# Optimization experiments

Measured on AMD Instinct MI355X. Metric: run time of the kernel, lower is better.

## Reference

```python
import jax, jax.numpy as jnp
import numpy as np

NEG = -1000000.0  # mask fill value used by the torch module

def setup_inputs() -> dict:
    key = jax.random.key(0)
    ks = jax.random.split(key, 7)
    B, Tq, Tk, Din, H, Dv = 16, 128, 256, 64, 256, 256
    return {
        "queries": jax.random.normal(ks[0], (B, Tq, Din), dtype=jnp.float32),
        "keys": jax.random.normal(ks[1], (B, Tk, Din), dtype=jnp.float32),
        "values": jax.random.normal(ks[2], (B, Tk, Dv), dtype=jnp.float32),
        "valid_lens": jax.random.randint(ks[3], (B,), 0, Tk, dtype=jnp.int32),
        "wq": jax.random.normal(ks[4], (Din, H), dtype=jnp.float32) * 0.05,
        "wk": jax.random.normal(ks[5], (Din, H), dtype=jnp.float32) * 0.05,
        "wv": jax.random.normal(ks[6], (H,), dtype=jnp.float32) * 0.05,
    }

def reference(queries, keys, values, valid_lens, wq, wk, wv):
    # Project queries and keys to num_hiddens
    q = jnp.einsum("bqd,dh->bqh", queries, wq)       # [B,Tq,H]
    k = jnp.einsum("bkd,dh->bkh", keys, wk)          # [B,Tk,H]
    # Additive features [B,Tq,Tk,H] -> tanh -> scalar score via wv
    feats = jnp.tanh(q[:, :, None, :] + k[:, None, :, :])
    scores = jnp.einsum("bqkh,h->bqk", feats, wv)    # [B,Tq,Tk]
    # Masked softmax over last axis; valid_lens [B] broadcasts over Tq
    Tk = scores.shape[-1]
    mask = jnp.arange(Tk)[None, None, :] < valid_lens[:, None, None]
    scores = jnp.where(mask, scores, NEG)
    attn = jax.nn.softmax(scores, axis=-1)           # [B,Tq,Tk]
    return jnp.einsum("bqk,bkv->bqv", attn, values)  # [B,Tq,Dv]
```

## Files before the change

kernel.cpp:

```cpp
#include <hip/hip_runtime.h>

#define B_  16
#define TQ  128
#define TK  256
#define DIN 64
#define H_  256
#define DV  256
#define HT  8
#define QT  4
#define NW  8
#define NEG -1000000.0f

#define SCALE  2.8853900817779268f
#define LOG2E  1.4426950408889634f

__device__ inline float fast_exp2(float x) { return __builtin_amdgcn_exp2f(x); }
__device__ inline float fast_rcp(float x)  { return __builtin_amdgcn_rcpf(x); }

__global__ __launch_bounds__(256) void proj_k_kernel(
    const float* __restrict__ keys, const float* __restrict__ wk,
    float* __restrict__ kpT, const int* __restrict__ valid_lens)
{
    int b  = blockIdx.x >> 5;
    int h0 = (blockIdx.x & 31) * HT;
    int t  = threadIdx.x;
    int vlC = (valid_lens[b] + 63) & ~63;
    if (t >= vlC) return;
    const float* krow = keys + (b * TK + t) * DIN;
    float acc[HT];
    #pragma unroll
    for (int hh = 0; hh < HT; ++hh) acc[hh] = 0.f;
    #pragma unroll 4
    for (int d = 0; d < DIN; ++d) {
        float kv = krow[d];
        #pragma unroll
        for (int hh = 0; hh < HT; ++hh)
            acc[hh] = fmaf(kv, wk[d * H_ + h0 + hh], acc[hh]);
    }
    #pragma unroll
    for (int hh = 0; hh < HT; ++hh)
        kpT[(b * H_ + h0 + hh) * TK + t] = acc[hh] * SCALE;
}

__device__ inline float waveMax(float v) {
    #pragma unroll
    for (int off = 32; off > 0; off >>= 1) v = fmaxf(v, __shfl_xor(v, off, 64));
    return v;
}
__device__ inline float waveSum(float v) {
    #pragma unroll
    for (int off = 32; off > 0; off >>= 1) v += __shfl_xor(v, off, 64);
    return v;
}

#define ROW4(qr, sacc)                                            \
    {                                                             \
        float u0 = (qr) + kv.x, u1 = (qr) + kv.y;                 \
        float u2 = (qr) + kv.z, u3 = (qr) + kv.w;                 \
        float r0 = fast_rcp(fast_exp2(u0) + 1.f);                 \
        float r1 = fast_rcp(fast_exp2(u1) + 1.f);                 \
        float r2 = fast_rcp(fast_exp2(u2) + 1.f);                 \
        float r3 = fast_rcp(fast_exp2(u3) + 1.f);                 \
        sacc.x = fmaf(wvh, fmaf(-2.f, r0, 1.f), sacc.x);          \
        sacc.y = fmaf(wvh, fmaf(-2.f, r1, 1.f), sacc.y);          \
        sacc.z = fmaf(wvh, fmaf(-2.f, r2, 1.f), sacc.z);          \
        sacc.w = fmaf(wvh, fmaf(-2.f, r3, 1.f), sacc.w);          \
    }

__global__ __launch_bounds__(512) void attn_kernel(
    const float* __restrict__ queries, const float* __restrict__ wq,
    const float* __restrict__ kpT,
    const float* __restrict__ values, const int* __restrict__ valid_lens,
    const float* __restrict__ wv, float* __restrict__ out)
{
    __shared__ float2 qs2[2][H_];
    __shared__ float  wvL[H_];
    __shared__ float  scoreP[NW][QT][TK];
    __shared__ float  attnT[TK][QT];

    int bx = blockIdx.x;
    int xcd = bx & 7;
    int i   = bx >> 3;
    int b   = xcd + 8 * (i & 1);
    int q0  = (i >> 1) * QT;
    int t   = threadIdx.x;
    int w   = t >> 6, l = t & 63;
    int vl  = valid_lens[b];

    {
        int h = t & 255, rp = t >> 8;
        const float* qbase = queries + (b * TQ + q0 + rp * 2) * DIN;
        float a0 = 0.f, a1 = 0.f;
        #pragma unroll
        for (int d = 0; d < DIN; ++d) {
            float ww = wq[d * H_ + h];
            a0 = fmaf(qbase[d],       ww, a0);
            a1 = fmaf(qbase[DIN + d], ww, a1);
        }
        qs2[rp][h] = make_float2(a0 * SCALE, a1 * SCALE);
        if (t < 256) wvL[h] = wv[h];
    }
    __syncthreads();

    {
        const float4* kp4 = (const float4*)(kpT + (size_t)b * H_ * TK);
        float4 s0 = {0,0,0,0}, s1 = {0,0,0,0}, s2 = {0,0,0,0}, s3 = {0,0,0,0};
        int h0 = w * (H_ / NW);
        #pragma unroll 2
        for (int hh = 0; hh < H_ / NW; ++hh) {
            int h = h0 + hh;
            float4 kv  = kp4[h * (TK / 4) + l];
            float2 qA  = qs2[0][h];
            float2 qB  = qs2[1][h];
            float  wvh = wvL[h];
            ROW4(qA.x, s0);
            ROW4(qA.y, s1);
            ROW4(qB.x, s2);
            ROW4(qB.y, s3);
        }
        ((float4*)&scoreP[w][0][0])[l] = s0;
        ((float4*)&scoreP[w][1][0])[l] = s1;
        ((float4*)&scoreP[w][2][0])[l] = s2;
        ((float4*)&scoreP[w][3][0])[l] = s3;
    }
    __syncthreads();

    if (t < 64 * QT) {
        int r = w;
        float4 v = {0,0,0,0};
        #pragma unroll
        for (int s = 0; s < NW; ++s) {
            float4 ps = ((const float4*)&scoreP[s][r][0])[l];
            v.x += ps.x; v.y += ps.y; v.z += ps.z; v.w += ps.w;
        }
        int k0 = 4 * l;
        v.x = (k0     < vl) ? v.x : NEG;
        v.y = (k0 + 1 < vl) ? v.y : NEG;
        v.z = (k0 + 2 < vl) ? v.z : NEG;
        v.w = (k0 + 3 < vl) ? v.w : NEG;
        float m  = waveMax(fmaxf(fmaxf(v.x, v.y), fmaxf(v.z, v.w)));
        float p0 = fast_exp2((v.x - m) * LOG2E);
        float p1 = fast_exp2((v.y - m) * LOG2E);
        float p2 = fast_exp2((v.z - m) * LOG2E);
        float p3 = fast_exp2((v.w - m) * LOG2E);
        float dr = fast_rcp(waveSum(p0 + p1 + p2 + p3));
        attnT[k0    ][r] = p0 * dr;
        attnT[k0 + 1][r] = p1 * dr;
        attnT[k0 + 2][r] = p2 * dr;
        attnT[k0 + 3][r] = p3 * dr;
    }
    __syncthreads();

    {
        int half = t >> 8, v = t & 255;
        int kLim = (vl == 0) ? TK : vl;
        int kBeg = half * (TK / 2);
        int kEnd = min(kBeg + TK / 2, kLim);
        const float*  vcol = values + (size_t)b * TK * DV + v;
        const float4* at4  = (const float4*)attnT;
        float o0 = 0.f, o1 = 0.f, o2 = 0.f, o3 = 0.f;
        #pragma unroll 4
        for (int k = kBeg; k < kEnd; ++k) {
            float  vv = vcol[k * DV];
            float4 a  = at4[k];
            o0 = fmaf(a.x, vv, o0);
            o1 = fmaf(a.y, vv, o1);
            o2 = fmaf(a.z, vv, o2);
            o3 = fmaf(a.w, vv, o3);
        }
        if (half == 1) {
            scoreP[0][0][v] = o0;
            scoreP[0][1][v] = o1;
            scoreP[0][2][v] = o2;
            scoreP[0][3][v] = o3;
        }
        __syncthreads();
        if (half == 0) {
            float* orow = out + (size_t)(b * TQ + q0) * DV + v;
            orow[0]      = o0 + scoreP[0][0][v];
            orow[DV]     = o1 + scoreP[0][1][v];
            orow[2 * DV] = o2 + scoreP[0][2][v];
            orow[3 * DV] = o3 + scoreP[0][3][v];
        }
    }
}

extern "C" void kernel_launch(void* const* d_in, const int* in_sizes, int n_in,
                              void* d_out, int out_size, void* d_ws, size_t ws_size,
                              hipStream_t stream) {
    const float* queries    = (const float*)d_in[0];
    const float* keys       = (const float*)d_in[1];
    const float* values     = (const float*)d_in[2];
    const int*   valid_lens = (const int*)  d_in[3];
    const float* wq         = (const float*)d_in[4];
    const float* wk         = (const float*)d_in[5];
    const float* wv         = (const float*)d_in[6];
    float* out = (float*)d_out;

    float* kpT = (float*)d_ws;

    proj_k_kernel<<<B_ * (H_ / HT), 256, 0, stream>>>(keys, wk, kpT, valid_lens);
    attn_kernel<<<B_ * (TQ / QT), 512, 0, stream>>>(queries, wq, kpT, values,
                                                    valid_lens, wv, out);
}
```

Before: 114.7 us.

## Halve query tile, hoist tanh affine terms out of inner loop, pack q/wv in LDS

Cuts the query tile per block from 4 rows to 2, which doubles the grid and lowers per-thread register pressure. It sets launch_bounds to (512, 8). The constant part of tanh(x)=1-2/(e^2x+1) is factored out: the inner loop now accumulates wv*rcp(...) only, and sum(wv) minus twice that sum is applied once per score before the mask. The projected query pair and wv are packed into one float4 per h in LDS. The trade-off is that kpT rows and the value matrix are now re-read by twice as many blocks, and half the threads sit idle during the query projection.

```diff
diff --git a/kernel.cpp b/kernel.cpp
--- a/kernel.cpp
+++ b/kernel.cpp
@@ -7,7 +7,7 @@
 #define H_  256
 #define DV  256
 #define HT  8
-#define QT  4
+#define QT  2
 #define NW  8
 #define NEG -1000000.0f
 
@@ -53,32 +53,17 @@
     return v;
 }
 
-#define ROW4(qr, sacc)                                            \
-    {                                                             \
-        float u0 = (qr) + kv.x, u1 = (qr) + kv.y;                 \
-        float u2 = (qr) + kv.z, u3 = (qr) + kv.w;                 \
-        float r0 = fast_rcp(fast_exp2(u0) + 1.f);                 \
-        float r1 = fast_rcp(fast_exp2(u1) + 1.f);                 \
-        float r2 = fast_rcp(fast_exp2(u2) + 1.f);                 \
-        float r3 = fast_rcp(fast_exp2(u3) + 1.f);                 \
-        sacc.x = fmaf(wvh, fmaf(-2.f, r0, 1.f), sacc.x);          \
-        sacc.y = fmaf(wvh, fmaf(-2.f, r1, 1.f), sacc.y);          \
-        sacc.z = fmaf(wvh, fmaf(-2.f, r2, 1.f), sacc.z);          \
-        sacc.w = fmaf(wvh, fmaf(-2.f, r3, 1.f), sacc.w);          \
-    }
-
-__global__ __launch_bounds__(512) void attn_kernel(
+__global__ __launch_bounds__(512, 8) void attn_kernel(
     const float* __restrict__ queries, const float* __restrict__ wq,
     const float* __restrict__ kpT,
     const float* __restrict__ values, const int* __restrict__ valid_lens,
     const float* __restrict__ wv, float* __restrict__ out)
 {
-    __shared__ float2 qs2[2][H_];
-    __shared__ float  wvL[H_];
+    __shared__ float4 qw4[H_];
     __shared__ float  scoreP[NW][QT][TK];
-    __shared__ float  attnT[TK][QT];
+    __shared__ float2 attnT[TK];
 
-    int bx = blockIdx.x;
+    int bx  = blockIdx.x;
     int xcd = bx & 7;
     int i   = bx >> 3;
     int b   = xcd + 8 * (i & 1);
@@ -87,67 +72,74 @@
     int w   = t >> 6, l = t & 63;
     int vl  = valid_lens[b];
 
-    {
-        int h = t & 255, rp = t >> 8;
-        const float* qbase = queries + (b * TQ + q0 + rp * 2) * DIN;
+    if (t < 256) {
+        const float* qbase = queries + (b * TQ + q0) * DIN;
         float a0 = 0.f, a1 = 0.f;
         #pragma unroll
         for (int d = 0; d < DIN; ++d) {
-            float ww = wq[d * H_ + h];
+            float ww = wq[d * H_ + t];
             a0 = fmaf(qbase[d],       ww, a0);
             a1 = fmaf(qbase[DIN + d], ww, a1);
         }
-        qs2[rp][h] = make_float2(a0 * SCALE, a1 * SCALE);
-        if (t < 256) wvL[h] = wv[h];
+        qw4[t] = make_float4(a0 * SCALE, a1 * SCALE, wv[t], 0.f);
     }
     __syncthreads();
 
     {
         const float4* kp4 = (const float4*)(kpT + (size_t)b * H_ * TK);
-        float4 s0 = {0,0,0,0}, s1 = {0,0,0,0}, s2 = {0,0,0,0}, s3 = {0,0,0,0};
+        float4 s0 = {0,0,0,0}, s1 = {0,0,0,0};
         int h0 = w * (H_ / NW);
-        #pragma unroll 2
+        #pragma unroll 4
         for (int hh = 0; hh < H_ / NW; ++hh) {
             int h = h0 + hh;
-            float4 kv  = kp4[h * (TK / 4) + l];
-            float2 qA  = qs2[0][h];
-            float2 qB  = qs2[1][h];
-            float  wvh = wvL[h];
-            ROW4(qA.x, s0);
-            ROW4(qA.y, s1);
-            ROW4(qB.x, s2);
-            ROW4(qB.y, s3);
+            float4 kv = kp4[h * (TK / 4) + l];
+            float4 qv = qw4[h];
+            float r0x = fast_rcp(fast_exp2(qv.x + kv.x) + 1.f);
+            float r0y = fast_rcp(fast_exp2(qv.x + kv.y) + 1.f);
+            float r0z = fast_rcp(fast_exp2(qv.x + kv.z) + 1.f);
+            float r0w = fast_rcp(fast_exp2(qv.x + kv.w) + 1.f);
+            s0.x = fmaf(qv.z, r0x, s0.x);
+            s0.y = fmaf(qv.z, r0y, s0.y);
+            s0.z = fmaf(qv.z, r0z, s0.z);
+            s0.w = fmaf(qv.z, r0w, s0.w);
+            float r1x = fast_rcp(fast_exp2(qv.y + kv.x) + 1.f);
+            float r1y = fast_rcp(fast_exp2(qv.y + kv.y) + 1.f);
+            float r1z = fast_rcp(fast_exp2(qv.y + kv.z) + 1.f);
+            float r1w = fast_rcp(fast_exp2(qv.y + kv.w) + 1.f);
+            s1.x = fmaf(qv.z, r1x, s1.x);
+            s1.y = fmaf(qv.z, r1y, s1.y);
+            s1.z = fmaf(qv.z, r1z, s1.z);
+            s1.w = fmaf(qv.z, r1w, s1.w);
         }
         ((float4*)&scoreP[w][0][0])[l] = s0;
         ((float4*)&scoreP[w][1][0])[l] = s1;
-        ((float4*)&scoreP[w][2][0])[l] = s2;
-        ((float4*)&scoreP[w][3][0])[l] = s3;
     }
     __syncthreads();
 
     if (t < 64 * QT) {
         int r = w;
-        float4 v = {0,0,0,0};
+        float W = waveSum(qw4[l].z + qw4[l + 64].z + qw4[l + 128].z + qw4[l + 192].z);
+        float4 v = {0, 0, 0, 0};
         #pragma unroll
         for (int s = 0; s < NW; ++s) {
             float4 ps = ((const float4*)&scoreP[s][r][0])[l];
             v.x += ps.x; v.y += ps.y; v.z += ps.z; v.w += ps.w;
         }
         int k0 = 4 * l;
-        v.x = (k0     < vl) ? v.x : NEG;
-        v.y = (k0 + 1 < vl) ? v.y : NEG;
-        v.z = (k0 + 2 < vl) ? v.z : NEG;
-        v.w = (k0 + 3 < vl) ? v.w : NEG;
+        v.x = (k0     < vl) ? fmaf(-2.f, v.x, W) : NEG;
+        v.y = (k0 + 1 < vl) ? fmaf(-2.f, v.y, W) : NEG;
+        v.z = (k0 + 2 < vl) ? fmaf(-2.f, v.z, W) : NEG;
+        v.w = (k0 + 3 < vl) ? fmaf(-2.f, v.w, W) : NEG;
         float m  = waveMax(fmaxf(fmaxf(v.x, v.y), fmaxf(v.z, v.w)));
         float p0 = fast_exp2((v.x - m) * LOG2E);
         float p1 = fast_exp2((v.y - m) * LOG2E);
         float p2 = fast_exp2((v.z - m) * LOG2E);
         float p3 = fast_exp2((v.w - m) * LOG2E);
         float dr = fast_rcp(waveSum(p0 + p1 + p2 + p3));
-        attnT[k0    ][r] = p0 * dr;
-        attnT[k0 + 1][r] = p1 * dr;
-        attnT[k0 + 2][r] = p2 * dr;
-        attnT[k0 + 3][r] = p3 * dr;
+        ((float*)&attnT[k0    ])[r] = p0 * dr;
+        ((float*)&attnT[k0 + 1])[r] = p1 * dr;
+        ((float*)&attnT[k0 + 2])[r] = p2 * dr;
+        ((float*)&attnT[k0 + 3])[r] = p3 * dr;
     }
     __syncthreads();
 
@@ -156,31 +148,24 @@
         int kLim = (vl == 0) ? TK : vl;
         int kBeg = half * (TK / 2);
         int kEnd = min(kBeg + TK / 2, kLim);
-        const float*  vcol = values + (size_t)b * TK * DV + v;
-        const float4* at4  = (const float4*)attnT;
-        float o0 = 0.f, o1 = 0.f, o2 = 0.f, o3 = 0.f;
+        const float* vcol = values + (size_t)b * TK * DV + v;
+        float o0 = 0.f, o1 = 0.f;
         #pragma unroll 4
         for (int k = kBeg; k < kEnd; ++k) {
             float  vv = vcol[k * DV];
-            float4 a  = at4[k];
+            float2 a  = attnT[k];
             o0 = fmaf(a.x, vv, o0);
             o1 = fmaf(a.y, vv, o1);
-            o2 = fmaf(a.z, vv, o2);
-            o3 = fmaf(a.w, vv, o3);
         }
         if (half == 1) {
             scoreP[0][0][v] = o0;
             scoreP[0][1][v] = o1;
-            scoreP[0][2][v] = o2;
-            scoreP[0][3][v] = o3;
         }
         __syncthreads();
         if (half == 0) {
             float* orow = out + (size_t)(b * TQ + q0) * DV + v;
-            orow[0]      = o0 + scoreP[0][0][v];
-            orow[DV]     = o1 + scoreP[0][1][v];
-            orow[2 * DV] = o2 + scoreP[0][2][v];
-            orow[3 * DV] = o3 + scoreP[0][3][v];
+            orow[0]  = o0 + scoreP[0][0][v];
+            orow[DV] = o1 + scoreP[0][1][v];
         }
     }
 }
```

After: 115.9 us. No clear change (+1.1%).

## Hoist tanh affine term out of hot loop, prefetch K rows, vectorize key loads

Applied to the files above, without the earlier changes.

The constant and -2 scale of tanh(x)=1-2/(1+e^{2x}) are pulled out of the inner score loop. The sum of wv is added once per score in the softmax stage, which saves two ops per element in the hottest loop. The key-projection loop now reads keys as float4, and the score loop software-prefetches the next kpT row. Launch bounds gain a minimum-blocks hint, which may constrain register allocation and cause spills, and factoring out the affine term slightly changes rounding.

```diff
diff --git a/kernel.cpp b/kernel.cpp
--- a/kernel.cpp
+++ b/kernel.cpp
@@ -26,16 +26,22 @@
     int t  = threadIdx.x;
     int vlC = (valid_lens[b] + 63) & ~63;
     if (t >= vlC) return;
-    const float* krow = keys + (b * TK + t) * DIN;
+    const float4* krow4 = (const float4*)(keys + (size_t)(b * TK + t) * DIN);
     float acc[HT];
     #pragma unroll
     for (int hh = 0; hh < HT; ++hh) acc[hh] = 0.f;
     #pragma unroll 4
-    for (int d = 0; d < DIN; ++d) {
-        float kv = krow[d];
-        #pragma unroll
-        for (int hh = 0; hh < HT; ++hh)
-            acc[hh] = fmaf(kv, wk[d * H_ + h0 + hh], acc[hh]);
+    for (int d4 = 0; d4 < DIN / 4; ++d4) {
+        float4 kd = krow4[d4];
+        const float* wrow = wk + 4 * d4 * H_ + h0;
+        #pragma unroll
+        for (int hh = 0; hh < HT; ++hh) acc[hh] = fmaf(kd.x, wrow[hh], acc[hh]);
+        #pragma unroll
+        for (int hh = 0; hh < HT; ++hh) acc[hh] = fmaf(kd.y, wrow[H_ + hh], acc[hh]);
+        #pragma unroll
+        for (int hh = 0; hh < HT; ++hh) acc[hh] = fmaf(kd.z, wrow[2 * H_ + hh], acc[hh]);
+        #pragma unroll
+        for (int hh = 0; hh < HT; ++hh) acc[hh] = fmaf(kd.w, wrow[3 * H_ + hh], acc[hh]);
     }
     #pragma unroll
     for (int hh = 0; hh < HT; ++hh)
@@ -53,21 +59,7 @@
     return v;
 }
 
-#define ROW4(qr, sacc)                                            \
-    {                                                             \
-        float u0 = (qr) + kv.x, u1 = (qr) + kv.y;                 \
-        float u2 = (qr) + kv.z, u3 = (qr) + kv.w;                 \
-        float r0 = fast_rcp(fast_exp2(u0) + 1.f);                 \
-        float r1 = fast_rcp(fast_exp2(u1) + 1.f);                 \
-        float r2 = fast_rcp(fast_exp2(u2) + 1.f);                 \
-        float r3 = fast_rcp(fast_exp2(u3) + 1.f);                 \
-        sacc.x = fmaf(wvh, fmaf(-2.f, r0, 1.f), sacc.x);          \
-        sacc.y = fmaf(wvh, fmaf(-2.f, r1, 1.f), sacc.y);          \
-        sacc.z = fmaf(wvh, fmaf(-2.f, r2, 1.f), sacc.z);          \
-        sacc.w = fmaf(wvh, fmaf(-2.f, r3, 1.f), sacc.w);          \
-    }
-
-__global__ __launch_bounds__(512) void attn_kernel(
+__global__ __launch_bounds__(512, 4) void attn_kernel(
     const float* __restrict__ queries, const float* __restrict__ wq,
     const float* __restrict__ kpT,
     const float* __restrict__ values, const int* __restrict__ valid_lens,
@@ -78,7 +70,7 @@
     __shared__ float  scoreP[NW][QT][TK];
     __shared__ float  attnT[TK][QT];
 
-    int bx = blockIdx.x;
+    int bx  = blockIdx.x;
     int xcd = bx & 7;
     int i   = bx >> 3;
     int b   = xcd + 8 * (i & 1);
@@ -89,7 +81,7 @@
 
     {
         int h = t & 255, rp = t >> 8;
-        const float* qbase = queries + (b * TQ + q0 + rp * 2) * DIN;
+        const float* qbase = queries + (size_t)(b * TQ + q0 + rp * 2) * DIN;
         float a0 = 0.f, a1 = 0.f;
         #pragma unroll
         for (int d = 0; d < DIN; ++d) {
@@ -106,18 +98,39 @@
         const float4* kp4 = (const float4*)(kpT + (size_t)b * H_ * TK);
         float4 s0 = {0,0,0,0}, s1 = {0,0,0,0}, s2 = {0,0,0,0}, s3 = {0,0,0,0};
         int h0 = w * (H_ / NW);
-        #pragma unroll 2
-        for (int hh = 0; hh < H_ / NW; ++hh) {
-            int h = h0 + hh;
-            float4 kv  = kp4[h * (TK / 4) + l];
+
+        auto body = [&](int h, float4 kv) {
             float2 qA  = qs2[0][h];
             float2 qB  = qs2[1][h];
             float  wvh = wvL[h];
-            ROW4(qA.x, s0);
-            ROW4(qA.y, s1);
-            ROW4(qB.x, s2);
-            ROW4(qB.y, s3);
-        }
+            float r;
+            r = fast_rcp(fast_exp2(qA.x + kv.x) + 1.f); s0.x = fmaf(wvh, r, s0.x);
+            r = fast_rcp(fast_exp2(qA.x + kv.y) + 1.f); s0.y = fmaf(wvh, r, s0.y);
+            r = fast_rcp(fast_exp2(qA.x + kv.z) + 1.f); s0.z = fmaf(wvh, r, s0.z);
+            r = fast_rcp(fast_exp2(qA.x + kv.w) + 1.f); s0.w = fmaf(wvh, r, s0.w);
+            r = fast_rcp(fast_exp2(qA.y + kv.x) + 1.f); s1.x = fmaf(wvh, r, s1.x);
+            r = fast_rcp(fast_exp2(qA.y + kv.y) + 1.f); s1.y = fmaf(wvh, r, s1.y);
+            r = fast_rcp(fast_exp2(qA.y + kv.z) + 1.f); s1.z = fmaf(wvh, r, s1.z);
+            r = fast_rcp(fast_exp2(qA.y + kv.w) + 1.f); s1.w = fmaf(wvh, r, s1.w);
+            r = fast_rcp(fast_exp2(qB.x + kv.x) + 1.f); s2.x = fmaf(wvh, r, s2.x);
+            r = fast_rcp(fast_exp2(qB.x + kv.y) + 1.f); s2.y = fmaf(wvh, r, s2.y);
+            r = fast_rcp(fast_exp2(qB.x + kv.z) + 1.f); s2.z = fmaf(wvh, r, s2.z);
+            r = fast_rcp(fast_exp2(qB.x + kv.w) + 1.f); s2.w = fmaf(wvh, r, s2.w);
+            r = fast_rcp(fast_exp2(qB.y + kv.x) + 1.f); s3.x = fmaf(wvh, r, s3.x);
+            r = fast_rcp(fast_exp2(qB.y + kv.y) + 1.f); s3.y = fmaf(wvh, r, s3.y);
+            r = fast_rcp(fast_exp2(qB.y + kv.z) + 1.f); s3.z = fmaf(wvh, r, s3.z);
+            r = fast_rcp(fast_exp2(qB.y + kv.w) + 1.f); s3.w = fmaf(wvh, r, s3.w);
+        };
+
+        float4 kv = kp4[(size_t)h0 * (TK / 4) + l];
+        #pragma unroll 2
+        for (int hh = 0; hh < H_ / NW - 1; ++hh) {
+            float4 kvn = kp4[(size_t)(h0 + hh + 1) * (TK / 4) + l];
+            body(h0 + hh, kv);
+            kv = kvn;
+        }
+        body(h0 + H_ / NW - 1, kv);
+
         ((float4*)&scoreP[w][0][0])[l] = s0;
         ((float4*)&scoreP[w][1][0])[l] = s1;
         ((float4*)&scoreP[w][2][0])[l] = s2;
@@ -127,17 +140,18 @@
 
     if (t < 64 * QT) {
         int r = w;
-        float4 v = {0,0,0,0};
+        float W = waveSum(wvL[l] + wvL[l + 64] + wvL[l + 128] + wvL[l + 192]);
+        float4 v = {0, 0, 0, 0};
         #pragma unroll
         for (int s = 0; s < NW; ++s) {
             float4 ps = ((const float4*)&scoreP[s][r][0])[l];
             v.x += ps.x; v.y += ps.y; v.z += ps.z; v.w += ps.w;
         }
         int k0 = 4 * l;
-        v.x = (k0     < vl) ? v.x : NEG;
-        v.y = (k0 + 1 < vl) ? v.y : NEG;
-        v.z = (k0 + 2 < vl) ? v.z : NEG;
-        v.w = (k0 + 3 < vl) ? v.w : NEG;
+        v.x = (k0     < vl) ? fmaf(-2.f, v.x, W) : NEG;
+        v.y = (k0 + 1 < vl) ? fmaf(-2.f, v.y, W) : NEG;
+        v.z = (k0 + 2 < vl) ? fmaf(-2.f, v.z, W) : NEG;
+        v.w = (k0 + 3 < vl) ? fmaf(-2.f, v.w, W) : NEG;
         float m  = waveMax(fmaxf(fmaxf(v.x, v.y), fmaxf(v.z, v.w)));
         float p0 = fast_exp2((v.x - m) * LOG2E);
         float p1 = fast_exp2((v.y - m) * LOG2E);
```

New measurement: 112.3 us. 1.02x faster.
